# Kernel optimization log

Measured on AMD Instinct MI355X. Metric: run time of the kernel, lower is better.

## Reference

```python
import jax, jax.numpy as jnp
import numpy as np

N, E, HS, HBS, L, SH, RBF, T, NZ, NH = 1024, 16384, 128, 32, 5, 25, 32, 50, 10, 4
HD = HS // NH
OUT = 14  # 3x0e + 2x1e + 1x2e -> 3 + 6 + 5
_rng = np.random.default_rng(7)
# fixed Clebsch-Gordan-style coupling tensor and expansion coefficients (deterministic constants)
CG = jnp.asarray((0.1 * _rng.normal(size=(SH, SH, SH))).astype(np.float32))
EXP = jnp.asarray((0.1 * _rng.normal(size=(SH, OUT, OUT))).astype(np.float32))
_SL = [(l * l, 2 * l + 1) for l in range(5)]  # per-l (offset, size) blocks in the 25-dim rep


def _real_sh(d):
    # real spherical harmonics l=0..4 of unit vectors d [E,3] -> [E,25]
    x, y, z = d[:, 0], d[:, 1], d[:, 2]
    x2, y2, z2 = x * x, y * y, z * z
    sh = [0.282095 * jnp.ones_like(x),
          0.488603 * y, 0.488603 * z, 0.488603 * x,
          1.092548 * x * y, 1.092548 * y * z, 0.315392 * (3 * z2 - 1), 1.092548 * x * z, 0.546274 * (x2 - y2),
          0.590044 * y * (3 * x2 - y2), 2.890611 * x * y * z, 0.457046 * y * (5 * z2 - 1),
          0.373176 * z * (5 * z2 - 3), 0.457046 * x * (5 * z2 - 1), 1.445306 * z * (x2 - y2),
          0.590044 * x * (x2 - 3 * y2),
          2.503343 * x * y * (x2 - y2), 1.770131 * y * z * (3 * x2 - y2), 0.946175 * x * y * (7 * z2 - 1),
          0.669047 * y * z * (7 * z2 - 3), 0.105786 * (35 * z2 * z2 - 30 * z2 + 3),
          0.669047 * x * z * (7 * z2 - 3), 0.473087 * (x2 - y2) * (7 * z2 - 1),
          1.770131 * x * z * (x2 - 3 * y2), 0.625836 * (x2 * x2 - 6 * x2 * y2 + y2 * y2)]
    return jnp.stack(sh, axis=-1)


def _rbf(r, cutoff=12.0, alpha=0.5):
    # exponential Bernstein radial basis with cosine cutoff, [E] -> [E,RBF]
    logf = np.concatenate([[0.0], np.cumsum(np.log(np.arange(1, RBF)))])
    logbinom = jnp.asarray((logf[RBF - 1] - logf - logf[::-1]).astype(np.float32))
    k = jnp.arange(RBF, dtype=jnp.float32)
    xr = jnp.exp(-alpha * r)[:, None]
    log1mx = jnp.log1p(-xr + 1e-7)
    b = jnp.exp(logbinom[None] + k[None] * (-alpha * r[:, None]) + (RBF - 1 - k)[None] * log1mx)
    fcut = 0.5 * (jnp.cos(jnp.pi * jnp.clip(r / cutoff, 0.0, 1.0)) + 1.0)
    return b * fcut[:, None]


def _mix(feat, W):
    # per-degree channel mixing: feat [*,C,25], W [5,C,D] -> [*,D,25]
    return jnp.concatenate([jnp.einsum('ncm,cd->ndm', feat[..., o:o + s], W[l])
                            for l, (o, s) in enumerate(_SL)], axis=-1)


def _forward(z, pos, edge_index, batch, t, step, embed, temb_T, temb_H, sig_W1, sig_b1, sig_W2, sig_b2,
             rad_W1, rad_b1, rad_W2, rad_b2, rad_W3, rad_b3, mix_W, Wq, Wk, Wii, Wij, path_ii, path_ij):
    n = z.shape[0]
    e = edge_index.shape[1]
    src, dst = edge_index[0], edge_index[1]
    vec = pos[src] - pos[dst]
    r = jnp.sqrt((vec * vec).sum(-1) + 1e-12)
    dvec = vec / r[:, None]
    rbf = _rbf(r)           # [E,32]
    sh = _real_sh(dvec)     # [E,25]
    nsc = embed[z]          # [N,HS]
    cat = jnp.concatenate([nsc, jnp.tile(temb_T[t][None], (n, 1)), jnp.tile(temb_H[step][None], (n, 1))], axis=-1)
    nsc = jax.nn.relu(cat @ sig_W1 + sig_b1) @ sig_W2 + sig_b2  # sigma_embedding
    x = jnp.zeros((n, HS, SH), jnp.float32).at[:, :, 0].set(nsc)  # scalar-initialized irrep features
    for l in range(L):
        # radial MLP -> per-edge per-channel tensor-product path weights
        h = jax.nn.silu(rbf @ rad_W1[l] + rad_b1[l])
        h = jax.nn.silu(h @ rad_W2[l] + rad_b2[l])
        w = h @ rad_W3[l] + rad_b3[l]                    # [E,HS]
        Tk = jnp.einsum('ej,ijk->eik', sh, CG)           # [E,25,25] CG-coupled SH operator
        msg = jnp.einsum('eci,eik->eck', x[src], Tk) * w[:, :, None]  # per-edge TP message [E,HS,25]
        agg = jax.ops.segment_sum(msg, dst, num_segments=n)
        y = _mix(agg, mix_W[l])
        # equivariant edge attention (scalars drive logits, full irreps are values)
        q = (x[:, :, 0] @ Wq[l]).reshape(n, NH, HD)
        kk = (x[:, :, 0] @ Wk[l]).reshape(n, NH, HD)
        logits = (q[dst] * kk[src]).sum(-1) * (1.0 / float(np.sqrt(HD)))  # [E,NH]
        m = jax.ops.segment_max(logits, dst, num_segments=n)
        m = jnp.where(jnp.isfinite(m), m, 0.0)
        a = jnp.exp(logits - m[dst])
        den = jax.ops.segment_sum(a, dst, num_segments=n)
        alpha = a / (den[dst] + 1e-9)
        v = x[src].reshape(e, NH, HD, SH)
        att = jax.ops.segment_sum(alpha[:, :, None, None] * v, dst, num_segments=n).reshape(n, HS, SH)
        x = x + y + att
        # gate nonlinearity: ssp/silu on scalars, sigmoid gate on higher-l blocks
        g = jax.nn.sigmoid(x[:, :, 0:1])
        x = jnp.concatenate([jax.nn.silu(x[:, :, 0:1]), x[:, :, 1:] * g], axis=-1)
    # expansion to hamiltonian blocks (3x0e+2x1e+1x2e -> 14x14)
    fii = _mix(x, Wii)                    # [N,HBS,25]
    fij = _mix(x[src] + x[dst], Wij)      # [E,HBS,25]
    w_ii = nsc @ path_ii                  # [N,HBS] path weights
    w_ij = jnp.concatenate([nsc[src], nsc[dst]], axis=-1) @ path_ij  # [E,HBS]
    H_ii = jnp.einsum('nd,ndm,mpq->npq', w_ii, fii, EXP)  # [N,14,14]
    H_ij = jnp.einsum('ed,edm,mpq->epq', w_ij, fij, EXP)  # [E,14,14]
    return H_ii, H_ij


def setup_inputs() -> dict:
    key = jax.random.key(0)
    ks = jax.random.split(key, 40)
    def nrm(i, shape, s):
        return (jax.random.normal(ks[i], shape) * s).astype(jnp.float32)
    inp = {}
    inp['z'] = jax.random.randint(ks[0], (N,), 0, NZ)
    inp['pos'] = nrm(1, (N, 3), 3.0)
    inp['edge_index'] = jax.random.randint(ks[2], (2, E), 0, N)
    inp['batch'] = jnp.sort(jax.random.randint(ks[3], (N,), 0, 8))
    inp['t'] = 25
    inp['step'] = 10
    inp['embed'] = nrm(4, (NZ, HS), 1.0)
    inp['temb_T'] = nrm(5, (T, HS), 1.0)
    inp['temb_H'] = nrm(6, (T, HS), 1.0)
    inp['sig_W1'] = nrm(7, (3 * HS, HS), (3 * HS) ** -0.5)
    inp['sig_b1'] = jnp.zeros((HS,), jnp.float32)
    inp['sig_W2'] = nrm(8, (HS, HS), HS ** -0.5)
    inp['sig_b2'] = jnp.zeros((HS,), jnp.float32)
    inp['rad_W1'] = nrm(9, (L, RBF, 64), RBF ** -0.5)
    inp['rad_b1'] = jnp.zeros((L, 64), jnp.float32)
    inp['rad_W2'] = nrm(10, (L, 64, 64), 64 ** -0.5)
    inp['rad_b2'] = jnp.zeros((L, 64), jnp.float32)
    inp['rad_W3'] = nrm(11, (L, 64, HS), 64 ** -0.5)
    inp['rad_b3'] = jnp.zeros((L, HS), jnp.float32)
    inp['mix_W'] = nrm(12, (L, 5, HS, HS), HS ** -0.5)
    inp['Wq'] = nrm(13, (L, HS, HS), HS ** -0.5)
    inp['Wk'] = nrm(14, (L, HS, HS), HS ** -0.5)
    inp['Wii'] = nrm(15, (5, HS, HBS), HS ** -0.5)
    inp['Wij'] = nrm(16, (5, HS, HBS), HS ** -0.5)
    inp['path_ii'] = nrm(17, (HS, HBS), HS ** -0.5)
    inp['path_ij'] = nrm(18, (2 * HS, HBS), (2 * HS) ** -0.5)
    return inp


def reference(z, pos, edge_index, batch, t, step, embed, temb_T, temb_H, sig_W1, sig_b1, sig_W2, sig_b2,
              rad_W1, rad_b1, rad_W2, rad_b2, rad_W3, rad_b3, mix_W, Wq, Wk, Wii, Wij, path_ii, path_ij):
    return _forward(z, pos, edge_index, batch, t, step, embed, temb_T, temb_H, sig_W1, sig_b1, sig_W2, sig_b2,
                    rad_W1, rad_b1, rad_W2, rad_b2, rad_W3, rad_b3, mix_W, Wq, Wk, Wii, Wij, path_ii, path_ij)
```

## Files before the change

### kernel.cpp

```cpp
#include <hip/hip_runtime.h>
#include <cstdint>
#include <cmath>
#include <cstddef>

constexpr int NN   = 1024;
constexpr int NE   = 16384;
constexpr int HSZ  = 128;
constexpr int NSH  = 25;
constexpr int NRBF = 32;
constexpr int NLAY = 5;
constexpr int XSZ  = HSZ * NSH;
constexpr int HII_SZ = NN * 196;


constexpr size_t OFF_CONSTS = 0;
constexpr size_t OFF_X    = 20560;
constexpr size_t OFF_AGG  = OFF_X    + (size_t)NN * XSZ;
constexpr size_t OFF_ATT  = OFF_AGG  + (size_t)NN * XSZ;
constexpr size_t OFF_X0   = OFF_ATT  + (size_t)NN * XSZ;
constexpr size_t OFF_NSC  = OFF_X0   + (size_t)NN * HSZ;
constexpr size_t OFF_Q    = OFF_NSC  + (size_t)NN * HSZ;
constexpr size_t OFF_K    = OFF_Q    + (size_t)NN * HSZ;
constexpr size_t OFF_RBF  = OFF_K    + (size_t)NN * HSZ;
constexpr size_t OFF_SH   = OFF_RBF  + (size_t)NE * NRBF;
constexpr size_t OFF_TK   = OFF_SH   + (size_t)NE * NSH;
constexpr size_t OFF_WRAD = OFF_TK   + (size_t)NE * NSH * NSH;
constexpr size_t OFF_INT  = OFF_WRAD + (size_t)NE * HSZ;
constexpr size_t NEED_BYTES = OFF_INT * 4 + (size_t)(1024 + 1025 + 1024 + 16384) * 4;

namespace qhc {

struct Pcg64 {
  unsigned __int128 state, inc;
  static unsigned __int128 mult() {
    return (((unsigned __int128)2549297995355413924ULL) << 64) | 4865540595714422341ULL;
  }
  void step() { state = state * mult() + inc; }
  uint64_t next64() {
    step();
    uint64_t hi = (uint64_t)(state >> 64), lo = (uint64_t)state;
    uint64_t x = hi ^ lo;
    unsigned rot = (unsigned)(state >> 122);
    return (x >> rot) | (x << ((64u - rot) & 63u));
  }
  double nextd() { return (double)(next64() >> 11) * (1.0 / 9007199254740992.0); }
};

struct HostConsts {
  float buf[20560];
  HostConsts() {
    const uint32_t INIT_A = 0x43b0d7e5u, MULT_A = 0x931e8875u;
    const uint32_t INIT_B = 0x8b51f9ddu, MULT_B = 0x58f38dedu;
    uint32_t pool[4];
    uint32_t hc = INIT_A;
    auto hashf = [&](uint32_t v) -> uint32_t {
      v ^= hc; hc *= MULT_A; v *= hc; v ^= v >> 16; return v;
    };
    auto mixf = [](uint32_t x, uint32_t y) -> uint32_t {
      uint32_t r = x * 0xca01f9ddu - y * 0x4973f715u;
      r ^= r >> 16;
      return r;
    };
    pool[0] = hashf(7u);
    for (int i = 1; i < 4; i++) pool[i] = hashf(0u);
    for (int s = 0; s < 4; s++)
      for (int d = 0; d < 4; d++)
        if (s != d) pool[d] = mixf(pool[d], hashf(pool[s]));
    uint32_t st32[8];
    uint32_t hb = INIT_B;
    for (int i = 0; i < 8; i++) {
      uint32_t v = pool[i % 4];
      v ^= hb; hb *= MULT_B; v *= hb; v ^= v >> 16;
      st32[i] = v;
    }
    uint64_t w0 = st32[0] | ((uint64_t)st32[1] << 32);
    uint64_t w1 = st32[2] | ((uint64_t)st32[3] << 32);
    uint64_t w2 = st32[4] | ((uint64_t)st32[5] << 32);
    uint64_t w3 = st32[6] | ((uint64_t)st32[7] << 32);
    unsigned __int128 seed = (((unsigned __int128)w0) << 64) | w1;
    unsigned __int128 incs = (((unsigned __int128)w2) << 64) | w3;
    Pcg64 g;
    g.state = 0; g.inc = (incs << 1) | 1;
    g.step(); g.state += seed; g.step();
    double wi[256], fi[256]; uint64_t ki[256];
    {
      const double m1 = 4503599627370496.0;
      double dn = 3.6541528853610087963519472518, tn = dn, vn = 0.00492867323399941;
      double q = vn / std::exp(-0.5 * dn * dn);
      ki[0] = (uint64_t)((dn / q) * m1); ki[1] = 0;
      wi[0] = q / m1; wi[255] = dn / m1;
      fi[0] = 1.0; fi[255] = std::exp(-0.5 * dn * dn);
      for (int i = 254; i >= 1; i--) {
        dn = std::sqrt(-2.0 * std::log(vn / dn + std::exp(-0.5 * dn * dn)));
        ki[i + 1] = (uint64_t)((dn / tn) * m1);
        tn = dn;
        fi[i] = std::exp(-0.5 * dn * dn);
        wi[i] = dn / m1;
      }
    }
    const double ZR = 3.6541528853610087963519472518;
    const double ZIR = 0.27366123732975827203338247596;
    auto stdnorm = [&]() -> double {
      for (;;) {
        uint64_t r = g.next64();
        int idx = (int)(r & 0xff);
        r >>= 8;
        int sign = (int)(r & 1);
        uint64_t rabs = (r >> 1) & 0x000fffffffffffffULL;
        double xv = (double)rabs * wi[idx];
        if (sign) xv = -xv;
        if (rabs < ki[idx]) return xv;
        if (idx == 0) {
          for (;;) {
            double xx = -ZIR * std::log1p(-g.nextd());
            double yy = -std::log1p(-g.nextd());
            if (yy + yy > xx * xx)
              return ((rabs >> 8) & 1) ? -(ZR + xx) : (ZR + xx);
          }
        } else {
          if (((fi[idx - 1] - fi[idx]) * g.nextd() + fi[idx]) < std::exp(-0.5 * xv * xv))
            return xv;
        }
      }
    };
    for (int i = 0; i < 15625 + 4900; i++) buf[i] = (float)(0.1 * stdnorm());
    double logf[32]; logf[0] = 0.0;
    for (int i = 1; i < 32; i++) logf[i] = logf[i - 1] + std::log((double)i);
    for (int k = 0; k < 32; k++) buf[15625 + 4900 + k] = (float)(logf[31] - logf[k] - logf[31 - k]);
    buf[20557] = buf[20558] = buf[20559] = 0.f;
  }
};
static HostConsts g_hc;
}

__device__ __forceinline__ float siluf(float a) { return a / (1.f + expf(-a)); }

__global__ __launch_bounds__(256) void qh_geom(
    const float* __restrict__ pos, const int* __restrict__ ei,
    const float* __restrict__ lbn, float* __restrict__ rbf, float* __restrict__ sh) {
  int e = blockIdx.x * 256 + threadIdx.x;
  if (e >= NE) return;
  int s = ei[e], d = ei[NE + e];
  float vx = pos[s * 3 + 0] - pos[d * 3 + 0];
  float vy = pos[s * 3 + 1] - pos[d * 3 + 1];
  float vz = pos[s * 3 + 2] - pos[d * 3 + 2];
  float r = sqrtf(vx * vx + vy * vy + vz * vz + 1e-12f);
  float inv = 1.0f / r;
  float x = vx * inv, y = vy * inv, z = vz * inv;
  float x2 = x * x, y2 = y * y, z2 = z * z;
  float* sp = sh + (size_t)e * NSH;
  sp[0] = 0.282095f;
  sp[1] = 0.488603f * y;
  sp[2] = 0.488603f * z;
  sp[3] = 0.488603f * x;
  sp[4] = 1.092548f * x * y;
  sp[5] = 1.092548f * y * z;
  sp[6] = 0.315392f * (3.f * z2 - 1.f);
  sp[7] = 1.092548f * x * z;
  sp[8] = 0.546274f * (x2 - y2);
  sp[9] = 0.590044f * y * (3.f * x2 - y2);
  sp[10] = 2.890611f * x * y * z;
  sp[11] = 0.457046f * y * (5.f * z2 - 1.f);
  sp[12] = 0.373176f * z * (5.f * z2 - 3.f);
  sp[13] = 0.457046f * x * (5.f * z2 - 1.f);
  sp[14] = 1.445306f * z * (x2 - y2);
  sp[15] = 0.590044f * x * (x2 - 3.f * y2);
  sp[16] = 2.503343f * x * y * (x2 - y2);
  sp[17] = 1.770131f * y * z * (3.f * x2 - y2);
  sp[18] = 0.946175f * x * y * (7.f * z2 - 1.f);
  sp[19] = 0.669047f * y * z * (7.f * z2 - 3.f);
  sp[20] = 0.105786f * (35.f * z2 * z2 - 30.f * z2 + 3.f);
  sp[21] = 0.669047f * x * z * (7.f * z2 - 3.f);
  sp[22] = 0.473087f * (x2 - y2) * (7.f * z2 - 1.f);
  sp[23] = 1.770131f * x * z * (x2 - 3.f * y2);
  sp[24] = 0.625836f * (x2 * x2 - 6.f * x2 * y2 + y2 * y2);
  float xr = expf(-0.5f * r);
  float l1 = log1pf(-xr + 1e-7f);
  float fc = 0.5f * (cosf(3.14159265358979323846f * fminf(r * (1.0f / 12.0f), 1.0f)) + 1.0f);
  float* rp = rbf + (size_t)e * NRBF;
  for (int k = 0; k < NRBF; k++) {
    float b = expf(lbn[k] + (float)k * (-0.5f * r) + (float)(NRBF - 1 - k) * l1);
    rp[k] = b * fc;
  }
}

__global__ __launch_bounds__(256) void qh_tk(
    const float* __restrict__ sh, const float* __restrict__ CG, float* __restrict__ Tk) {
  __shared__ float shl[32 * NSH];
  int e0 = blockIdx.x * 32;
  int t = threadIdx.x;
  for (int i = t; i < 32 * NSH; i += 256) shl[i] = sh[(size_t)e0 * NSH + i];
  __syncthreads();
  for (int ik = t; ik < NSH * NSH; ik += 256) {
    int i = ik / NSH, k = ik % NSH;
    float cg[NSH];
#pragma unroll
    for (int j = 0; j < NSH; j++) cg[j] = CG[i * 625 + j * NSH + k];
    for (int ee = 0; ee < 32; ee++) {
      float acc = 0.f;
#pragma unroll
      for (int j = 0; j < NSH; j++) acc += shl[ee * NSH + j] * cg[j];
      Tk[(size_t)(e0 + ee) * 625 + ik] = acc;
    }
  }
}

__global__ __launch_bounds__(128) void qh_nsc(
    const int* __restrict__ z, const int* __restrict__ tptr, const int* __restrict__ sptr,
    const float* __restrict__ embed, const float* __restrict__ tT, const float* __restrict__ tH,
    const float* __restrict__ W1, const float* __restrict__ b1,
    const float* __restrict__ W2, const float* __restrict__ b2,
    float* __restrict__ nsc, float* __restrict__ x, float* __restrict__ x0) {
  __shared__ float cat[384];
  __shared__ float h[128];
  int nd = blockIdx.x, d = threadIdx.x;
  int zz = z[nd], tt = tptr[0], st = sptr[0];
  cat[d] = embed[zz * HSZ + d];
  cat[128 + d] = tT[tt * HSZ + d];
  cat[256 + d] = tH[st * HSZ + d];
  __syncthreads();
  float a = b1[d];
  for (int c = 0; c < 384; c++) a += cat[c] * W1[c * HSZ + d];
  h[d] = fmaxf(a, 0.f);
  __syncthreads();
  a = b2[d];
  for (int c = 0; c < 128; c++) a += h[c] * W2[c * HSZ + d];
  nsc[nd * HSZ + d] = a;
  x0[nd * HSZ + d] = a;
  float* xr = x + (size_t)nd * XSZ + d;
  xr[0] = a;
  for (int m = 1; m < NSH; m++) xr[m * 128] = 0.f;
}

__global__ __launch_bounds__(256) void qh_zero(int* counts) {
  int i = blockIdx.x * 256 + threadIdx.x;
  if (i < NN) counts[i] = 0;
}
__global__ __launch_bounds__(256) void qh_count(const int* __restrict__ ei, int* counts) {
  int e = blockIdx.x * 256 + threadIdx.x;
  if (e < NE) atomicAdd(&counts[ei[NE + e]], 1);
}
__global__ __launch_bounds__(1024) void qh_scan(const int* __restrict__ counts,
                                                int* starts, int* cursor) {
  __shared__ int tmp[NN];
  int t = threadIdx.x;
  tmp[t] = counts[t];
  __syncthreads();
  for (int ofs = 1; ofs < NN; ofs <<= 1) {
    int v = (t >= ofs) ? tmp[t - ofs] : 0;
    __syncthreads();
    tmp[t] += v;
    __syncthreads();
  }
  starts[t + 1] = tmp[t];
  if (t == 0) starts[0] = 0;
  cursor[t] = (t == 0) ? 0 : tmp[t - 1];
}
__global__ __launch_bounds__(256) void qh_scatter(const int* __restrict__ ei,
                                                  int* cursor, int* perm) {
  int e = blockIdx.x * 256 + threadIdx.x;
  if (e < NE) {
    int d = ei[NE + e];
    int pos = atomicAdd(&cursor[d], 1);
    perm[pos] = e;
  }
}

__global__ __launch_bounds__(256) void qh_rad(
    const float* __restrict__ rbf,
    const float* __restrict__ W1, const float* __restrict__ b1,
    const float* __restrict__ W2, const float* __restrict__ b2,
    const float* __restrict__ W3, const float* __restrict__ b3,
    float* __restrict__ wrad) {
  __shared__ float w1l[2048], w2l[4096], w3l[8192];
  __shared__ float rl[4][32], h1[4][64], h2[4][64];
  int t = threadIdx.x;
  for (int i = t; i < 2048; i += 256) w1l[i] = W1[i];
  for (int i = t; i < 4096; i += 256) w2l[i] = W2[i];
  for (int i = t; i < 8192; i += 256) w3l[i] = W3[i];
  __syncthreads();
  int e0 = blockIdx.x * 16;
  for (int q = 0; q < 4; q++) {
    int eb = e0 + q * 4;
    if (t < 128) rl[t >> 5][t & 31] = rbf[(size_t)(eb + (t >> 5)) * NRBF + (t & 31)];
    __syncthreads();
    {
      int eg = t >> 6, u = t & 63;
      float a = b1[u];
      for (int c = 0; c < 32; c++) a += rl[eg][c] * w1l[c * 64 + u];
      h1[eg][u] = siluf(a);
    }
    __syncthreads();
    {
      int eg = t >> 6, u = t & 63;
      float a = b2[u];
      for (int c = 0; c < 64; c++) a += h1[eg][c] * w2l[c * 64 + u];
      h2[eg][u] = siluf(a);
    }
    __syncthreads();
#pragma unroll
    for (int p = 0; p < 2; p++) {
      int eg = (t >> 7) + p * 2, u = t & 127;
      float a = b3[u];
      for (int c = 0; c < 64; c++) a += h2[eg][c] * w3l[c * 128 + u];
      wrad[(size_t)(eb + eg) * HSZ + u] = a;
    }
    __syncthreads();
  }
}

__global__ __launch_bounds__(256) void qh_qk(
    const float* __restrict__ x0, const float* __restrict__ Wq, const float* __restrict__ Wk,
    float* __restrict__ q, float* __restrict__ kk) {
  __shared__ float xl[128];
  int nd = blockIdx.x, t = threadIdx.x;
  if (t < 128) xl[t] = x0[nd * HSZ + t];
  __syncthreads();
  int d = t & 127;
  const float* W = (t < 128) ? Wq : Wk;
  float a = 0.f;
  for (int c = 0; c < 128; c++) a += xl[c] * W[c * HSZ + d];
  if (t < 128) q[nd * HSZ + d] = a;
  else kk[nd * HSZ + d] = a;
}

__global__ __launch_bounds__(256) void qh_logit(
    const float* __restrict__ q, const float* __restrict__ kk,
    const int* __restrict__ ei, float* __restrict__ logits) {
  int t = threadIdx.x;
  int e = blockIdx.x * 2 + (t >> 7);
  int c = t & 127;
  int s = ei[e], d = ei[NE + e];
  float p = q[d * HSZ + c] * kk[s * HSZ + c];
#pragma unroll
  for (int m = 16; m >= 1; m >>= 1) p += __shfl_xor(p, m);
  if ((c & 31) == 0) logits[e * 4 + (c >> 5)] = p * 0.17677669529663687f;
}

__global__ __launch_bounds__(64) void qh_soft(
    const float* __restrict__ logits, const int* __restrict__ starts,
    const int* __restrict__ perm, float* __restrict__ alpha) {
  int nd = blockIdx.x, t = threadIdx.x;
  int hh = t >> 4, l = t & 15;
  int jb = starts[nd], je = starts[nd + 1];
  float m = -1e30f;
  for (int j = jb + l; j < je; j += 16) m = fmaxf(m, logits[perm[j] * 4 + hh]);
#pragma unroll
  for (int s = 1; s < 16; s <<= 1) m = fmaxf(m, __shfl_xor(m, s));
  float den = 0.f;
  for (int j = jb + l; j < je; j += 16) den += expf(logits[perm[j] * 4 + hh] - m);
#pragma unroll
  for (int s = 1; s < 16; s <<= 1) den += __shfl_xor(den, s);
  float inv = 1.f / (den + 1e-9f);
  for (int j = jb + l; j < je; j += 16) {
    int e = perm[j];
    alpha[e * 4 + hh] = expf(logits[e * 4 + hh] - m) * inv;
  }
}

__global__ __launch_bounds__(256) void qh_msgatt(
    const float* __restrict__ x, const float* __restrict__ Tk,
    const float* __restrict__ wrad, const float* __restrict__ alpha,
    const int* __restrict__ starts, const int* __restrict__ perm,
    const int* __restrict__ ei,
    float* __restrict__ agg, float* __restrict__ att) {
  __shared__ float xs[2][1600];
  __shared__ float tkl[2][628];
  __shared__ float wl[2][64];
  int nd = blockIdx.x >> 1, h = blockIdx.x & 1;
  int t = threadIdx.x;
  int cl = t & 63, q4 = t >> 6;
  int c = h * 64 + cl;
  int k0 = (q4 == 0) ? 0 : (1 + 6 * q4);
  int nk = (q4 == 0) ? 7 : 6;
  float am[7], aa[7];
#pragma unroll
  for (int u = 0; u < 7; u++) { am[u] = 0.f; aa[u] = 0.f; }
  int jb = starts[nd], je = starts[nd + 1];
  float rx[7], rt[3], rw = 0.f;
  if (jb < je) {
    int e = perm[jb], s = ei[e];
#pragma unroll
    for (int u = 0; u < 6; u++) {
      int i = t + u * 256;
      rx[u] = x[(size_t)s * XSZ + (i >> 6) * 128 + h * 64 + (i & 63)];
    }
    if (t < 64) rx[6] = x[(size_t)s * XSZ + 24 * 128 + h * 64 + t];
    rt[0] = Tk[(size_t)e * 625 + t];
    rt[1] = Tk[(size_t)e * 625 + 256 + t];
    if (t < 113) rt[2] = Tk[(size_t)e * 625 + 512 + t];
    if (t < 64) rw = wrad[(size_t)e * HSZ + h * 64 + t];
#pragma unroll
    for (int u = 0; u < 6; u++) xs[0][t + u * 256] = rx[u];
    if (t < 64) xs[0][1536 + t] = rx[6];
    tkl[0][t] = rt[0];
    tkl[0][256 + t] = rt[1];
    if (t < 113) tkl[0][512 + t] = rt[2];
    if (t < 64) wl[0][t] = rw;
  }
  __syncthreads();
  for (int j = jb; j < je; j++) {
    int cur = (j - jb) & 1, nxt = cur ^ 1;
    int e = perm[j];
    float al = alpha[e * 4 + (c >> 5)];
    bool more = (j + 1 < je);
    if (more) {
      int e2 = perm[j + 1], s2 = ei[e2];
#pragma unroll
      for (int u = 0; u < 6; u++) {
        int i = t + u * 256;
        rx[u] = x[(size_t)s2 * XSZ + (i >> 6) * 128 + h * 64 + (i & 63)];
      }
      if (t < 64) rx[6] = x[(size_t)s2 * XSZ + 24 * 128 + h * 64 + t];
      rt[0] = Tk[(size_t)e2 * 625 + t];
      rt[1] = Tk[(size_t)e2 * 625 + 256 + t];
      if (t < 113) rt[2] = Tk[(size_t)e2 * 625 + 512 + t];
      if (t < 64) rw = wrad[(size_t)e2 * HSZ + h * 64 + t];
    }
    float wc = wl[cur][cl];
#pragma unroll
    for (int i = 0; i < NSH; i++) {
      float xw = xs[cur][i * 64 + cl] * wc;
      const float* tr = &tkl[cur][i * 25 + k0];
#pragma unroll
      for (int u = 0; u < 7; u++)
        if (u < nk) am[u] += xw * tr[u];
    }
#pragma unroll
    for (int u = 0; u < 7; u++)
      if (u < nk) aa[u] += al * xs[cur][(k0 + u) * 64 + cl];
    __syncthreads();
    if (more) {
#pragma unroll
      for (int u = 0; u < 6; u++) xs[nxt][t + u * 256] = rx[u];
      if (t < 64) xs[nxt][1536 + t] = rx[6];
      tkl[nxt][t] = rt[0];
      tkl[nxt][256 + t] = rt[1];
      if (t < 113) tkl[nxt][512 + t] = rt[2];
      if (t < 64) wl[nxt][t] = rw;
    }
    __syncthreads();
  }
#pragma unroll
  for (int u = 0; u < 7; u++)
    if (u < nk) {
      agg[(size_t)nd * XSZ + (k0 + u) * 128 + c] = am[u];
      att[(size_t)nd * XSZ + (k0 + u) * 128 + c] = aa[u];
    }
}

__global__ __launch_bounds__(256) void qh_mixgemm(
    const float* __restrict__ mixW, float* __restrict__ agg) {
  __shared__ float Wl[8192];
  __shared__ float Al[4096];
  int b = blockIdx.x, t = threadIdx.x;
  int lb, cum;
  if (b < 32)       { lb = 0; cum = 0; }
  else if (b < 128) { lb = 1; cum = 32; }
  else if (b < 288) { lb = 2; cum = 128; }
  else if (b < 512) { lb = 3; cum = 288; }
  else              { lb = 4; cum = 512; }
  int sl = 2 * lb + 1, o = lb * lb;
  int row0 = (b - cum) * 32;
  const float* W = mixW + lb * 16384;
  for (int i = t; i < 4096; i += 256) {
    int r = i >> 7, cc = i & 127;
    int gr = row0 + r, n = gr / sl, m = o + gr - n * sl;
    Al[i] = agg[(size_t)n * XSZ + m * 128 + cc];
  }
  int dl = t & 63, rg = t >> 6;
  float out[2][8];
  for (int p = 0; p < 2; p++) {
    __syncthreads();
    for (int i = t; i < 8192; i += 256) {
      int cc = i >> 6, d2 = i & 63;
      Wl[i] = W[cc * 128 + p * 64 + d2];
    }
    __syncthreads();
    float acc[8];
#pragma unroll
    for (int r = 0; r < 8; r++) acc[r] = 0.f;
    for (int cc = 0; cc < 128; cc++) {
      float w = Wl[cc * 64 + dl];
#pragma unroll
      for (int r = 0; r < 8; r++) acc[r] += Al[(rg * 8 + r) * 128 + cc] * w;
    }
#pragma unroll
    for (int r = 0; r < 8; r++) out[p][r] = acc[r];
  }
#pragma unroll
  for (int p = 0; p < 2; p++)
#pragma unroll
    for (int r = 0; r < 8; r++) {
      int gr = row0 + rg * 8 + r, n = gr / sl, m = o + gr - n * sl;
      agg[(size_t)n * XSZ + m * 128 + p * 64 + dl] = out[p][r];
    }
}

__global__ __launch_bounds__(256) void qh_gate(
    const float* __restrict__ y, const float* __restrict__ att,
    float* __restrict__ x, float* __restrict__ x0) {
  __shared__ float v0l[128];
  int nd = blockIdx.x, t = threadIdx.x;
  int d = t & 127, mh = t >> 7;
  int m0 = mh ? 13 : 0, nm = mh ? 12 : 13;
  float v[13];
  size_t base = (size_t)nd * XSZ + (size_t)m0 * 128 + d;
#pragma unroll
  for (int u = 0; u < 13; u++)
    if (u < nm) v[u] = x[base + (size_t)u * 128] + y[base + (size_t)u * 128] + att[base + (size_t)u * 128];
  if (mh == 0) v0l[d] = v[0];
  __syncthreads();
  float g = 1.f / (1.f + expf(-v0l[d]));
#pragma unroll
  for (int u = 0; u < 13; u++)
    if (u < nm) x[base + (size_t)u * 128] = v[u] * g;
  if (mh == 0) x0[nd * HSZ + d] = v[0] * g;
}

__global__ __launch_bounds__(256) void qh_prep(
    const float* __restrict__ x, const float* __restrict__ nsc,
    const float* __restrict__ Wii, const float* __restrict__ Wij,
    const float* __restrict__ pii, const float* __restrict__ pij,
    const float* __restrict__ EXPc,
    float* __restrict__ fm, float* __restrict__ awb, float* __restrict__ out) {
  __shared__ float xl[XSZ];
  __shared__ float nl[128];
  __shared__ float wc[4096];
  __shared__ float fml[800];
  __shared__ float wiil[32];
  __shared__ float gl[25];
  int nd = blockIdx.x, t = threadIdx.x;
  for (int i = t; i < XSZ; i += 256) xl[i] = x[(size_t)nd * XSZ + i];
  if (t < 128) nl[t] = nsc[nd * HSZ + t];
  __syncthreads();
  if (t < 32) {
    float a = 0.f;
    for (int cc = 0; cc < 128; cc++) a += nl[cc] * pii[cc * 32 + t];
    wiil[t] = a;
  } else if (t < 96) {
    int d = (t - 32) & 31;
    int half = (t - 32) >> 5;
    const float* pp = pij + (half ? 128 * 32 : 0);
    float a = 0.f;
    for (int cc = 0; cc < 128; cc++) a += nl[cc] * pp[cc * 32 + d];
    awb[nd * 64 + half * 32 + d] = a;
  }
  for (int lb = 0; lb < 5; lb++) {
    __syncthreads();
    for (int i = t; i < 4096; i += 256) wc[i] = Wii[lb * 4096 + i];
    __syncthreads();
    int o = lb * lb, sl = 2 * lb + 1;
    for (int idx = t; idx < 32 * sl; idx += 256) {
      int d = idx & 31, m = o + (idx >> 5);
      float a = 0.f;
      for (int cc = 0; cc < 128; cc++) a += xl[m * 128 + cc] * wc[cc * 32 + d];
      fml[d * NSH + m] = a;
    }
  }
  __syncthreads();
  if (t < 25) {
    float a = 0.f;
#pragma unroll
    for (int d = 0; d < 32; d++) a += wiil[d] * fml[d * NSH + t];
    gl[t] = a;
  }
  __syncthreads();
  if (t < 196) {
    float a = 0.f;
#pragma unroll
    for (int m = 0; m < 25; m++) a += gl[m] * EXPc[m * 196 + t];
    out[(size_t)nd * 196 + t] = a;
  }
  for (int lb = 0; lb < 5; lb++) {
    __syncthreads();
    for (int i = t; i < 4096; i += 256) wc[i] = Wij[lb * 4096 + i];
    __syncthreads();
    int o = lb * lb, sl = 2 * lb + 1;
    for (int idx = t; idx < 32 * sl; idx += 256) {
      int d = idx & 31, m = o + (idx >> 5);
      float a = 0.f;
      for (int cc = 0; cc < 128; cc++) a += xl[m * 128 + cc] * wc[cc * 32 + d];
      fm[(size_t)nd * 800 + d * NSH + m] = a;
    }
  }
}

__global__ __launch_bounds__(256) void qh_fij2(
    const int* __restrict__ ei, const float* __restrict__ fm,
    const float* __restrict__ awb, const float* __restrict__ EXPc,
    float* __restrict__ out) {
  __shared__ float fsum[800], wsum[32], gl[25];
  int e = blockIdx.x, t = threadIdx.x;
  int s = ei[e], d2 = ei[NE + e];
  for (int i = t; i < 800; i += 256)
    fsum[i] = fm[(size_t)s * 800 + i] + fm[(size_t)d2 * 800 + i];
  if (t < 32) wsum[t] = awb[s * 64 + t] + awb[d2 * 64 + 32 + t];
  __syncthreads();
  if (t < 25) {
    float a = 0.f;
#pragma unroll
    for (int d = 0; d < 32; d++) a += wsum[d] * fsum[d * NSH + t];
    gl[t] = a;
  }
  __syncthreads();
  if (t < 196) {
    float a = 0.f;
#pragma unroll
    for (int m = 0; m < 25; m++) a += gl[m] * EXPc[m * 196 + t];
    out[HII_SZ + (size_t)e * 196 + t] = a;
  }
}

extern "C" void kernel_launch(void* const* d_in, const int* in_sizes, int n_in,
                              void* d_out, int out_size, void* d_ws, size_t ws_size,
                              hipStream_t stream) {
  (void)in_sizes; (void)n_in; (void)out_size;
  if (ws_size < NEED_BYTES) return;

  const int*   z    = (const int*)d_in[0];
  const float* pos  = (const float*)d_in[1];
  const int*   ei   = (const int*)d_in[2];
  const int*   tptr = (const int*)d_in[4];
  const int*   sptr = (const int*)d_in[5];
  const float* embed= (const float*)d_in[6];
  const float* tT   = (const float*)d_in[7];
  const float* tH   = (const float*)d_in[8];
  const float* sW1  = (const float*)d_in[9];
  const float* sb1  = (const float*)d_in[10];
  const float* sW2  = (const float*)d_in[11];
  const float* sb2  = (const float*)d_in[12];
  const float* rW1  = (const float*)d_in[13];
  const float* rb1  = (const float*)d_in[14];
  const float* rW2  = (const float*)d_in[15];
  const float* rb2  = (const float*)d_in[16];
  const float* rW3  = (const float*)d_in[17];
  const float* rb3  = (const float*)d_in[18];
  const float* mixW = (const float*)d_in[19];
  const float* Wq   = (const float*)d_in[20];
  const float* Wk   = (const float*)d_in[21];
  const float* Wii  = (const float*)d_in[22];
  const float* Wij  = (const float*)d_in[23];
  const float* pii  = (const float*)d_in[24];
  const float* pij  = (const float*)d_in[25];

  float* ws = (float*)d_ws;
  float* CGd   = ws + OFF_CONSTS;
  float* EXPd  = CGd + 15625;
  float* LBNd  = CGd + 15625 + 4900;
  float* x     = ws + OFF_X;
  float* agg   = ws + OFF_AGG;
  float* att   = ws + OFF_ATT;
  float* x0    = ws + OFF_X0;
  float* nsc   = ws + OFF_NSC;
  float* qarr  = ws + OFF_Q;
  float* karr  = ws + OFF_K;
  float* rbf   = ws + OFF_RBF;
  float* sh    = ws + OFF_SH;
  float* Tk    = ws + OFF_TK;
  float* wrad  = ws + OFF_WRAD;
  float* logits = ws + OFF_SH;
  float* alphaA = ws + OFF_SH + 65536;
  float* fm     = ws + OFF_AGG;
  float* awb    = ws + OFF_AGG + 819200;
  int* ibase   = (int*)(ws + OFF_INT);
  int* counts  = ibase;
  int* starts  = ibase + 1024;
  int* cursor  = ibase + 1024 + 1025;
  int* perm    = ibase + 1024 + 1025 + 1024;
  float* outp  = (float*)d_out;

  hipMemcpyAsync(CGd, qhc::g_hc.buf, 20557 * sizeof(float), hipMemcpyHostToDevice, stream);

  qh_geom<<<NE / 256, 256, 0, stream>>>(pos, ei, LBNd, rbf, sh);
  qh_tk<<<NE / 32, 256, 0, stream>>>(sh, CGd, Tk);
  qh_nsc<<<NN, 128, 0, stream>>>(z, tptr, sptr, embed, tT, tH, sW1, sb1, sW2, sb2, nsc, x, x0);
  qh_zero<<<NN / 256, 256, 0, stream>>>(counts);
  qh_count<<<NE / 256, 256, 0, stream>>>(ei, counts);
  qh_scan<<<1, 1024, 0, stream>>>(counts, starts, cursor);
  qh_scatter<<<NE / 256, 256, 0, stream>>>(ei, cursor, perm);

  for (int l = 0; l < NLAY; l++) {
    qh_rad<<<NE / 16, 256, 0, stream>>>(rbf,
        rW1 + (size_t)l * 32 * 64, rb1 + (size_t)l * 64,
        rW2 + (size_t)l * 64 * 64, rb2 + (size_t)l * 64,
        rW3 + (size_t)l * 64 * 128, rb3 + (size_t)l * 128, wrad);
    qh_qk<<<NN, 256, 0, stream>>>(x0, Wq + (size_t)l * 16384, Wk + (size_t)l * 16384, qarr, karr);
    qh_logit<<<NE / 2, 256, 0, stream>>>(qarr, karr, ei, logits);
    qh_soft<<<NN, 64, 0, stream>>>(logits, starts, perm, alphaA);
    qh_msgatt<<<NN * 2, 256, 0, stream>>>(x, Tk, wrad, alphaA, starts, perm, ei, agg, att);
    qh_mixgemm<<<800, 256, 0, stream>>>(mixW + (size_t)l * 81920, agg);
    qh_gate<<<NN, 256, 0, stream>>>(agg, att, x, x0);
  }

  qh_prep<<<NN, 256, 0, stream>>>(x, nsc, Wii, Wij, pii, pij, EXPd, fm, awb, outp);
  qh_fij2<<<NE, 256, 0, stream>>>(ei, fm, awb, EXPd, outp);
}
```

Baseline: 1.480 ms.

## Process two edges per iteration in message-attention kernel with deeper prefetch

The per-node edge loop in the message/attention kernel now handles two edges per iteration. Global loads for the next pair are issued before the current pair is computed, which halves the number of barrier pairs per edge. Edge indices and source nodes are staged in shared memory up front, and attention weights go through shared memory instead of a per-thread global read each step. The cost is roughly double the prefetch registers, which may reduce occupancy.

Measured after the change: 1.531 ms. +3.4%, slower.

```diff
diff --git a/kernel.cpp b/kernel.cpp
--- a/kernel.cpp
+++ b/kernel.cpp
@@ -367,86 +367,100 @@
   __shared__ float xs[2][1600];
   __shared__ float tkl[2][628];
   __shared__ float wl[2][64];
+  __shared__ float alb[2][4];
+  __shared__ int   eidx[64];
+  __shared__ int   esrc[64];
   int nd = blockIdx.x >> 1, h = blockIdx.x & 1;
   int t = threadIdx.x;
   int cl = t & 63, q4 = t >> 6;
   int c = h * 64 + cl;
+  int hd = c >> 5;
   int k0 = (q4 == 0) ? 0 : (1 + 6 * q4);
   int nk = (q4 == 0) ? 7 : 6;
   float am[7], aa[7];
 #pragma unroll
   for (int u = 0; u < 7; u++) { am[u] = 0.f; aa[u] = 0.f; }
   int jb = starts[nd], je = starts[nd + 1];
-  float rx[7], rt[3], rw = 0.f;
-  if (jb < je) {
-    int e = perm[jb], s = ei[e];
-#pragma unroll
-    for (int u = 0; u < 6; u++) {
-      int i = t + u * 256;
-      rx[u] = x[(size_t)s * XSZ + (i >> 6) * 128 + h * 64 + (i & 63)];
-    }
-    if (t < 64) rx[6] = x[(size_t)s * XSZ + 24 * 128 + h * 64 + t];
-    rt[0] = Tk[(size_t)e * 625 + t];
-    rt[1] = Tk[(size_t)e * 625 + 256 + t];
-    if (t < 113) rt[2] = Tk[(size_t)e * 625 + 512 + t];
-    if (t < 64) rw = wrad[(size_t)e * HSZ + h * 64 + t];
-#pragma unroll
-    for (int u = 0; u < 6; u++) xs[0][t + u * 256] = rx[u];
-    if (t < 64) xs[0][1536 + t] = rx[6];
-    tkl[0][t] = rt[0];
-    tkl[0][256 + t] = rt[1];
-    if (t < 113) tkl[0][512 + t] = rt[2];
-    if (t < 64) wl[0][t] = rw;
-  }
-  __syncthreads();
-  for (int j = jb; j < je; j++) {
-    int cur = (j - jb) & 1, nxt = cur ^ 1;
-    int e = perm[j];
-    float al = alpha[e * 4 + (c >> 5)];
-    bool more = (j + 1 < je);
-    if (more) {
-      int e2 = perm[j + 1], s2 = ei[e2];
-#pragma unroll
-      for (int u = 0; u < 6; u++) {
-        int i = t + u * 256;
-        rx[u] = x[(size_t)s2 * XSZ + (i >> 6) * 128 + h * 64 + (i & 63)];
-      }
-      if (t < 64) rx[6] = x[(size_t)s2 * XSZ + 24 * 128 + h * 64 + t];
-      rt[0] = Tk[(size_t)e2 * 625 + t];
-      rt[1] = Tk[(size_t)e2 * 625 + 256 + t];
-      if (t < 113) rt[2] = Tk[(size_t)e2 * 625 + 512 + t];
-      if (t < 64) rw = wrad[(size_t)e2 * HSZ + h * 64 + t];
-    }
-    float wc = wl[cur][cl];
-#pragma unroll
-    for (int i = 0; i < NSH; i++) {
-      float xw = xs[cur][i * 64 + cl] * wc;
-      const float* tr = &tkl[cur][i * 25 + k0];
-#pragma unroll
-      for (int u = 0; u < 7; u++)
-        if (u < nk) am[u] += xw * tr[u];
-    }
-#pragma unroll
-    for (int u = 0; u < 7; u++)
-      if (u < nk) aa[u] += al * xs[cur][(k0 + u) * 64 + cl];
-    __syncthreads();
-    if (more) {
-#pragma unroll
-      for (int u = 0; u < 6; u++) xs[nxt][t + u * 256] = rx[u];
-      if (t < 64) xs[nxt][1536 + t] = rx[6];
-      tkl[nxt][t] = rt[0];
-      tkl[nxt][256 + t] = rt[1];
-      if (t < 113) tkl[nxt][512 + t] = rt[2];
-      if (t < 64) wl[nxt][t] = rw;
-    }
-    __syncthreads();
-  }
+  int cnt = je - jb;
+  if (t < cnt && t < 64) {
+    int e = perm[jb + t];
+    eidx[t] = e;
+    esrc[t] = ei[e];
+  }
+  __syncthreads();
+
+#define QH_LOADR(p, rx, rt, rw, ra)                                         \
+  {                                                                         \
+    int e2 = ((p) < 64) ? eidx[p] : perm[jb + (p)];                         \
+    int s2 = ((p) < 64) ? esrc[p] : ei[e2];                                 \
+    _Pragma("unroll") for (int u = 0; u < 6; u++) {                         \
+      int i = t + u * 256;                                                  \
+      rx[u] = x[(size_t)s2 * XSZ + (i >> 6) * 128 + h * 64 + (i & 63)];     \
+    }                                                                       \
+    if (t < 64) rx[6] = x[(size_t)s2 * XSZ + 24 * 128 + h * 64 + t];        \
+    rt[0] = Tk[(size_t)e2 * 625 + t];                                       \
+    rt[1] = Tk[(size_t)e2 * 625 + 256 + t];                                 \
+    if (t < 113) rt[2] = Tk[(size_t)e2 * 625 + 512 + t];                    \
+    if (t < 64) rw = wrad[(size_t)e2 * HSZ + h * 64 + t];                   \
+    if (t < 4) ra = alpha[e2 * 4 + t];                                      \
+  }
+
+#define QH_WRITER(b, rx, rt, rw, ra)                                        \
+  {                                                                         \
+    _Pragma("unroll") for (int u = 0; u < 6; u++) xs[b][t + u * 256] = rx[u]; \
+    if (t < 64) xs[b][1536 + t] = rx[6];                                    \
+    tkl[b][t] = rt[0];                                                      \
+    tkl[b][256 + t] = rt[1];                                                \
+    if (t < 113) tkl[b][512 + t] = rt[2];                                   \
+    if (t < 64) wl[b][t] = rw;                                              \
+    if (t < 4) alb[b][t] = ra;                                              \
+  }
+
+#define QH_COMPUTE(b)                                                       \
+  {                                                                         \
+    float wc = wl[b][cl];                                                   \
+    float al = alb[b][hd];                                                  \
+    _Pragma("unroll") for (int i = 0; i < NSH; i++) {                       \
+      float xw = xs[b][i * 64 + cl] * wc;                                   \
+      const float* tr = &tkl[b][i * 25 + k0];                               \
+      _Pragma("unroll") for (int u = 0; u < 7; u++)                         \
+        if (u < nk) am[u] += xw * tr[u];                                    \
+    }                                                                       \
+    _Pragma("unroll") for (int u = 0; u < 7; u++)                           \
+      if (u < nk) aa[u] += al * xs[b][(k0 + u) * 64 + cl];                  \
+  }
+
+  {
+    float rx[7], rt[3], rw = 0.f, ra = 0.f;
+    if (cnt > 0) { QH_LOADR(0, rx, rt, rw, ra); QH_WRITER(0, rx, rt, rw, ra); }
+    if (cnt > 1) { QH_LOADR(1, rx, rt, rw, ra); QH_WRITER(1, rx, rt, rw, ra); }
+  }
+  __syncthreads();
+
+  float rxA[7], rtA[3], rwA = 0.f, raA = 0.f;
+  float rxB[7], rtB[3], rwB = 0.f, raB = 0.f;
+  for (int j0 = 0; j0 < cnt; j0 += 2) {
+    bool two = (j0 + 1 < cnt);
+    bool mA = (j0 + 2 < cnt), mB = (j0 + 3 < cnt);
+    if (mA) QH_LOADR(j0 + 2, rxA, rtA, rwA, raA);
+    if (mB) QH_LOADR(j0 + 3, rxB, rtB, rwB, raB);
+    QH_COMPUTE(0);
+    if (two) QH_COMPUTE(1);
+    __syncthreads();
+    if (mA) QH_WRITER(0, rxA, rtA, rwA, raA);
+    if (mB) QH_WRITER(1, rxB, rtB, rwB, raB);
+    __syncthreads();
+  }
+
 #pragma unroll
   for (int u = 0; u < 7; u++)
     if (u < nk) {
       agg[(size_t)nd * XSZ + (k0 + u) * 128 + c] = am[u];
       att[(size_t)nd * XSZ + (k0 + u) * 128 + c] = aa[u];
     }
+#undef QH_LOADR
+#undef QH_WRITER
+#undef QH_COMPUTE
 }
 
 __global__ __launch_bounds__(256) void qh_mixgemm(
```

## Pad Tk into per-wave aligned slots and read it as wave-uniform float4 loads

Applied to the files above, without the earlier changes.

The per-edge coupling tensor Tk is now written in a padded 800-float layout. Each wave's group of 6 or 7 output components sits in an aligned 8-float slot per input index. The message kernel reads these directly from global memory with wave-uniform float4 loads (readfirstlane on the edge index and wave id), replacing the shared-memory staging of Tk, and adds an occupancy hint to launch_bounds. This removes LDS traffic and the conditional inner loop, but grows the Tk buffer, adds a zero-fill in qh_tk, and makes every edge iteration issue global/scalar loads.

New measurement: 1.353 ms. 1.09x faster.

```diff
diff --git a/kernel.cpp b/kernel.cpp
--- a/kernel.cpp
+++ b/kernel.cpp
@@ -11,6 +11,7 @@
 constexpr int NLAY = 5;
 constexpr int XSZ  = HSZ * NSH;
 constexpr int HII_SZ = NN * 196;
+constexpr int TKP  = 800;
 
 
 constexpr size_t OFF_CONSTS = 0;
@@ -24,7 +25,7 @@
 constexpr size_t OFF_RBF  = OFF_K    + (size_t)NN * HSZ;
 constexpr size_t OFF_SH   = OFF_RBF  + (size_t)NE * NRBF;
 constexpr size_t OFF_TK   = OFF_SH   + (size_t)NE * NSH;
-constexpr size_t OFF_WRAD = OFF_TK   + (size_t)NE * NSH * NSH;
+constexpr size_t OFF_WRAD = OFF_TK   + (size_t)NE * TKP;
 constexpr size_t OFF_INT  = OFF_WRAD + (size_t)NE * HSZ;
 constexpr size_t NEED_BYTES = OFF_INT * 4 + (size_t)(1024 + 1025 + 1024 + 16384) * 4;
 
@@ -185,14 +186,16 @@
 }
 
 __global__ __launch_bounds__(256) void qh_tk(
-    const float* __restrict__ sh, const float* __restrict__ CG, float* __restrict__ Tk) {
+    const float* __restrict__ sh, const float* __restrict__ CG, float* __restrict__ Tkp) {
   __shared__ float shl[32 * NSH];
   int e0 = blockIdx.x * 32;
   int t = threadIdx.x;
   for (int i = t; i < 32 * NSH; i += 256) shl[i] = sh[(size_t)e0 * NSH + i];
+  for (int i = t; i < 32 * TKP; i += 256) Tkp[(size_t)e0 * TKP + i] = 0.f;
   __syncthreads();
   for (int ik = t; ik < NSH * NSH; ik += 256) {
     int i = ik / NSH, k = ik % NSH;
+    int pos = i * 32 + k + (k >= 7) + 2 * (k >= 13) + 2 * (k >= 19);
     float cg[NSH];
 #pragma unroll
     for (int j = 0; j < NSH; j++) cg[j] = CG[i * 625 + j * NSH + k];
@@ -200,7 +203,7 @@
       float acc = 0.f;
 #pragma unroll
       for (int j = 0; j < NSH; j++) acc += shl[ee * NSH + j] * cg[j];
-      Tk[(size_t)(e0 + ee) * 625 + ik] = acc;
+      Tkp[(size_t)(e0 + ee) * TKP + pos] = acc;
     }
   }
 }
@@ -358,18 +361,18 @@
   }
 }
 
-__global__ __launch_bounds__(256) void qh_msgatt(
-    const float* __restrict__ x, const float* __restrict__ Tk,
+__global__ __launch_bounds__(256, 8) void qh_msgatt(
+    const float* __restrict__ x, const float* __restrict__ Tkp,
     const float* __restrict__ wrad, const float* __restrict__ alpha,
     const int* __restrict__ starts, const int* __restrict__ perm,
     const int* __restrict__ ei,
     float* __restrict__ agg, float* __restrict__ att) {
   __shared__ float xs[2][1600];
-  __shared__ float tkl[2][628];
   __shared__ float wl[2][64];
   int nd = blockIdx.x >> 1, h = blockIdx.x & 1;
   int t = threadIdx.x;
   int cl = t & 63, q4 = t >> 6;
+  int q4u = __builtin_amdgcn_readfirstlane(q4);
   int c = h * 64 + cl;
   int k0 = (q4 == 0) ? 0 : (1 + 6 * q4);
   int nk = (q4 == 0) ? 7 : 6;
@@ -377,7 +380,8 @@
 #pragma unroll
   for (int u = 0; u < 7; u++) { am[u] = 0.f; aa[u] = 0.f; }
   int jb = starts[nd], je = starts[nd + 1];
-  float rx[7], rt[3], rw = 0.f;
+
+  float rx[7], rw = 0.f;
   if (jb < je) {
     int e = perm[jb], s = ei[e];
 #pragma unroll
@@ -386,22 +390,18 @@
       rx[u] = x[(size_t)s * XSZ + (i >> 6) * 128 + h * 64 + (i & 63)];
     }
     if (t < 64) rx[6] = x[(size_t)s * XSZ + 24 * 128 + h * 64 + t];
-    rt[0] = Tk[(size_t)e * 625 + t];
-    rt[1] = Tk[(size_t)e * 625 + 256 + t];
-    if (t < 113) rt[2] = Tk[(size_t)e * 625 + 512 + t];
     if (t < 64) rw = wrad[(size_t)e * HSZ + h * 64 + t];
 #pragma unroll
     for (int u = 0; u < 6; u++) xs[0][t + u * 256] = rx[u];
     if (t < 64) xs[0][1536 + t] = rx[6];
-    tkl[0][t] = rt[0];
-    tkl[0][256 + t] = rt[1];
-    if (t < 113) tkl[0][512 + t] = rt[2];
     if (t < 64) wl[0][t] = rw;
   }
   __syncthreads();
   for (int j = jb; j < je; j++) {
     int cur = (j - jb) & 1, nxt = cur ^ 1;
     int e = perm[j];
+    int eu = __builtin_amdgcn_readfirstlane(e);
+    const float* tkr = Tkp + (size_t)eu * TKP + q4u * 8;
     float al = alpha[e * 4 + (c >> 5)];
     bool more = (j + 1 < je);
     if (more) {
@@ -412,19 +412,16 @@
         rx[u] = x[(size_t)s2 * XSZ + (i >> 6) * 128 + h * 64 + (i & 63)];
       }
       if (t < 64) rx[6] = x[(size_t)s2 * XSZ + 24 * 128 + h * 64 + t];
-      rt[0] = Tk[(size_t)e2 * 625 + t];
-      rt[1] = Tk[(size_t)e2 * 625 + 256 + t];
-      if (t < 113) rt[2] = Tk[(size_t)e2 * 625 + 512 + t];
       if (t < 64) rw = wrad[(size_t)e2 * HSZ + h * 64 + t];
     }
     float wc = wl[cur][cl];
-#pragma unroll
+#pragma unroll 5
     for (int i = 0; i < NSH; i++) {
       float xw = xs[cur][i * 64 + cl] * wc;
-      const float* tr = &tkl[cur][i * 25 + k0];
-#pragma unroll
-      for (int u = 0; u < 7; u++)
-        if (u < nk) am[u] += xw * tr[u];
+      float4 t0 = *(const float4*)(tkr + i * 32);
+      float4 t1 = *(const float4*)(tkr + i * 32 + 4);
+      am[0] += xw * t0.x; am[1] += xw * t0.y; am[2] += xw * t0.z; am[3] += xw * t0.w;
+      am[4] += xw * t1.x; am[5] += xw * t1.y; am[6] += xw * t1.z;
     }
 #pragma unroll
     for (int u = 0; u < 7; u++)
@@ -434,9 +431,6 @@
 #pragma unroll
       for (int u = 0; u < 6; u++) xs[nxt][t + u * 256] = rx[u];
       if (t < 64) xs[nxt][1536 + t] = rx[6];
-      tkl[nxt][t] = rt[0];
-      tkl[nxt][256 + t] = rt[1];
-      if (t < 113) tkl[nxt][512 + t] = rt[2];
       if (t < 64) wl[nxt][t] = rw;
     }
     __syncthreads();
@@ -657,7 +651,7 @@
   float* karr  = ws + OFF_K;
   float* rbf   = ws + OFF_RBF;
   float* sh    = ws + OFF_SH;
-  float* Tk    = ws + OFF_TK;
+  float* Tkp   = ws + OFF_TK;
   float* wrad  = ws + OFF_WRAD;
   float* logits = ws + OFF_SH;
   float* alphaA = ws + OFF_SH + 65536;
@@ -673,7 +667,7 @@
   hipMemcpyAsync(CGd, qhc::g_hc.buf, 20557 * sizeof(float), hipMemcpyHostToDevice, stream);
 
   qh_geom<<<NE / 256, 256, 0, stream>>>(pos, ei, LBNd, rbf, sh);
-  qh_tk<<<NE / 32, 256, 0, stream>>>(sh, CGd, Tk);
+  qh_tk<<<NE / 32, 256, 0, stream>>>(sh, CGd, Tkp);
   qh_nsc<<<NN, 128, 0, stream>>>(z, tptr, sptr, embed, tT, tH, sW1, sb1, sW2, sb2, nsc, x, x0);
   qh_zero<<<NN / 256, 256, 0, stream>>>(counts);
   qh_count<<<NE / 256, 256, 0, stream>>>(ei, counts);
@@ -688,7 +682,7 @@
     qh_qk<<<NN, 256, 0, stream>>>(x0, Wq + (size_t)l * 16384, Wk + (size_t)l * 16384, qarr, karr);
     qh_logit<<<NE / 2, 256, 0, stream>>>(qarr, karr, ei, logits);
     qh_soft<<<NN, 64, 0, stream>>>(logits, starts, perm, alphaA);
-    qh_msgatt<<<NN * 2, 256, 0, stream>>>(x, Tk, wrad, alphaA, starts, perm, ei, agg, att);
+    qh_msgatt<<<NN * 2, 256, 0, stream>>>(x, Tkp, wrad, alphaA, starts, perm, ei, agg, att);
     qh_mixgemm<<<800, 256, 0, stream>>>(mixW + (size_t)l * 81920, agg);
     qh_gate<<<NN, 256, 0, stream>>>(agg, att, x, x0);
   }
```
